# Optimization experiments

Measured on AMD Instinct MI355X. Metric: run time of the kernel, lower is better.

The kernel has to match this reference:

```python
import jax, jax.numpy as jnp
import numpy as np

B, S, HID, H = 1, 2048, 512, 8
D = HID // H            # head_dim = 64
N_TIP, N_FAC = 16, 256
SCALE = 1.0 / np.sqrt(D).astype(np.float32)


def _dominant_dim_indices():
    # dominant_fcs = arange(n_tip) % (head_dim//2), identical for every head
    pair_dim = max(1, D // 2)
    fc = jnp.arange(N_TIP) % pair_dim                      # [n_tip]
    dim_idx = jnp.stack((fc * 2, fc * 2 + 1), axis=-1).reshape(-1)  # [2*n_tip]
    return jnp.clip(dim_idx, 0, D - 1)


def setup_inputs() -> dict:
    key = jax.random.key(0)
    kx, kq, kk, kv, ko = jax.random.split(key, 5)
    s = 1.0 / np.sqrt(HID)
    return {
        "x": jax.random.normal(kx, (B, S, HID), jnp.float32),
        "wq": jax.random.normal(kq, (HID, HID), jnp.float32) * s,
        "wk": jax.random.normal(kk, (HID, HID), jnp.float32) * s,
        "wv": jax.random.normal(kv, (HID, HID), jnp.float32) * s,
        "wo": jax.random.normal(ko, (HID, HID), jnp.float32) * s,
    }


def reference(x, wq, wk, wv, wo):
    # projections (nn.Linear, no bias): y = x @ W.T; split into heads -> [B,H,S,D]
    def split_heads(y):
        return y.reshape(B, S, H, D).transpose(0, 2, 1, 3)

    q = split_heads(x @ wq.T)
    k = split_heads(x @ wk.T)
    v = split_heads(x @ wv.T)

    dim_idx = _dominant_dim_indices()                      # [2*n_tip]
    q_sub = q[..., dim_idx]                                # [B,H,S,2*n_tip]
    k_sub = k[..., dim_idx]
    importance = jnp.einsum("bhqf,bhkf->bhqk", q_sub, k_sub)  # [B,H,S,S]

    n_sel = min(N_FAC, S)
    _, top_idx = jax.lax.top_k(importance, n_sel)          # [B,H,S,n_sel]

    # gather selected K/V per query: [B,H,S,n_sel,D]
    k_sel = jnp.take_along_axis(k[:, :, None], top_idx[..., None], axis=3)
    v_sel = jnp.take_along_axis(v[:, :, None], top_idx[..., None], axis=3)

    scores = jnp.einsum("bhqd,bhqkd->bhqk", q, k_sel) * SCALE
    attn = jax.nn.softmax(scores, axis=-1)
    out = jnp.einsum("bhqk,bhqkd->bhqd", attn, v_sel)      # [B,H,S,D]

    out = out.transpose(0, 2, 1, 3).reshape(B, S, HID)
    return out @ wo.T
```

## Files before the change

### kernel.cpp

```cpp
#include <hip/hip_runtime.h>

#define S_LEN  2048
#define HIDDEN 512
#define NHEAD  8
#define DHEAD  64
#define NSEL   256
#define ROWS_A 8
#define SCALE_ 0.125f

#define WAVE_SYNC() __asm__ volatile("s_waitcnt lgkmcnt(0)" ::: "memory")

__device__ __forceinline__ unsigned mapu(float f) {
  unsigned u = __float_as_uint(f);
  return (u & 0x80000000u) ? ~u : (u | 0x80000000u);
}

union H4 { _Float16 h[4]; uint2 u2; };

__device__ __forceinline__ void gemm_nt_body(const float* __restrict__ A,
                                             const float* __restrict__ B,
                                             float* __restrict__ C,
                                             int K, int N, int m0, int n0,
                                             float (*As)[68], float (*Bs)[68]) {
  const int t  = threadIdx.x;
  const int tx = t & 15, ty = t >> 4;
  const int rr = t >> 3, cc = (t & 7) << 2;
  float acc[4][4] = {};

  float4 fa0 = *(const float4*)&A[(size_t)(m0 + rr)      * K + cc];
  float4 fa1 = *(const float4*)&A[(size_t)(m0 + rr + 32) * K + cc];
  float4 fb0 = *(const float4*)&B[(size_t)(n0 + rr)      * K + cc];
  float4 fb1 = *(const float4*)&B[(size_t)(n0 + rr + 32) * K + cc];

  for (int k0 = 0; k0 < K; k0 += 32) {
    __syncthreads();
    As[cc + 0][rr] = fa0.x; As[cc + 1][rr] = fa0.y; As[cc + 2][rr] = fa0.z; As[cc + 3][rr] = fa0.w;
    As[cc + 0][rr + 32] = fa1.x; As[cc + 1][rr + 32] = fa1.y; As[cc + 2][rr + 32] = fa1.z; As[cc + 3][rr + 32] = fa1.w;
    Bs[cc + 0][rr] = fb0.x; Bs[cc + 1][rr] = fb0.y; Bs[cc + 2][rr] = fb0.z; Bs[cc + 3][rr] = fb0.w;
    Bs[cc + 0][rr + 32] = fb1.x; Bs[cc + 1][rr + 32] = fb1.y; Bs[cc + 2][rr + 32] = fb1.z; Bs[cc + 3][rr + 32] = fb1.w;
    __syncthreads();
    if (k0 + 32 < K) {
      fa0 = *(const float4*)&A[(size_t)(m0 + rr)      * K + k0 + 32 + cc];
      fa1 = *(const float4*)&A[(size_t)(m0 + rr + 32) * K + k0 + 32 + cc];
      fb0 = *(const float4*)&B[(size_t)(n0 + rr)      * K + k0 + 32 + cc];
      fb1 = *(const float4*)&B[(size_t)(n0 + rr + 32) * K + k0 + 32 + cc];
    }
#pragma unroll
    for (int kk = 0; kk < 32; ++kk) {
      const float4 a4 = *(const float4*)&As[kk][ty * 4];
      const float4 b4 = *(const float4*)&Bs[kk][tx * 4];
      const float a[4] = {a4.x, a4.y, a4.z, a4.w};
      const float b[4] = {b4.x, b4.y, b4.z, b4.w};
#pragma unroll
      for (int i = 0; i < 4; ++i)
#pragma unroll
        for (int j = 0; j < 4; ++j) acc[i][j] += a[i] * b[j];
    }
  }
#pragma unroll
  for (int i = 0; i < 4; ++i) {
    float4 o = make_float4(acc[i][0], acc[i][1], acc[i][2], acc[i][3]);
    *(float4*)&C[(size_t)(m0 + ty * 4 + i) * N + n0 + tx * 4] = o;
  }
}

__global__ __launch_bounds__(256) void gemm_nt(const float* __restrict__ A,
                                               const float* __restrict__ B,
                                               float* __restrict__ C,
                                               int M, int N, int K) {
  __shared__ float As[32][68];
  __shared__ float Bs[32][68];
  gemm_nt_body(A, B, C, K, N, blockIdx.x * 64, blockIdx.y * 64, As, Bs);
}

__global__ __launch_bounds__(256) void gemm_qkv(const float* __restrict__ x,
                                                const float* __restrict__ wq,
                                                const float* __restrict__ wk,
                                                const float* __restrict__ wv,
                                                float* __restrict__ Qb,
                                                float* __restrict__ Kb,
                                                float* __restrict__ Vb) {
  __shared__ float As[32][68];
  __shared__ float Bs[32][68];
  const int z = blockIdx.z;
  const float* B = (z == 0) ? wq : (z == 1) ? wk : wv;
  float*       C = (z == 0) ? Qb : (z == 1) ? Kb : Vb;
  gemm_nt_body(x, B, C, HIDDEN, HIDDEN, blockIdx.x * 64, blockIdx.y * 64, As, Bs);
}

__global__ __launch_bounds__(256) void score_gemm(const float* __restrict__ Q,
                                                  const float* __restrict__ K,
                                                  unsigned* __restrict__ impu,
                                                  _Float16* __restrict__ sch) {
  __shared__ float Qs[64][132];
  __shared__ float Ks[64][68];
  const int bid  = blockIdx.x;
  const int h    = bid & (NHEAD - 1);
  const int tile = bid >> 3;
  const int q0   = (tile & 15) * 128;
  const int k0   = (tile >> 4) * 64;
  const int t  = threadIdx.x;
  const int tx = t & 15, ty = t >> 4;

#pragma unroll
  for (int s = 0; s < 8; ++s) {
    const int sf = s * 256 + t;
    const int r = sf >> 4, c = (sf & 15) * 4;
    const float4 f = *(const float4*)&Q[(size_t)(q0 + r) * HIDDEN + h * DHEAD + c];
    Qs[c + 0][r] = f.x; Qs[c + 1][r] = f.y; Qs[c + 2][r] = f.z; Qs[c + 3][r] = f.w;
  }
#pragma unroll
  for (int s = 0; s < 4; ++s) {
    const int sf = s * 256 + t;
    const int r = sf >> 4, c = (sf & 15) * 4;
    const float4 f = *(const float4*)&K[(size_t)(k0 + r) * HIDDEN + h * DHEAD + c];
    Ks[c + 0][r] = f.x; Ks[c + 1][r] = f.y; Ks[c + 2][r] = f.z; Ks[c + 3][r] = f.w;
  }
  __syncthreads();

  float acc[8][4] = {};
#pragma unroll
  for (int d = 0; d < 32; ++d) {
    const float4 aa = *(const float4*)&Qs[d][ty * 8];
    const float4 ab = *(const float4*)&Qs[d][ty * 8 + 4];
    const float4 b4 = *(const float4*)&Ks[d][tx * 4];
    const float a[8] = {aa.x, aa.y, aa.z, aa.w, ab.x, ab.y, ab.z, ab.w};
    const float b[4] = {b4.x, b4.y, b4.z, b4.w};
#pragma unroll
    for (int i = 0; i < 8; ++i)
#pragma unroll
      for (int j = 0; j < 4; ++j) acc[i][j] += a[i] * b[j];
  }
  float simp[8][4];
#pragma unroll
  for (int i = 0; i < 8; ++i)
#pragma unroll
    for (int j = 0; j < 4; ++j) simp[i][j] = acc[i][j];
#pragma unroll
  for (int d = 32; d < 64; ++d) {
    const float4 aa = *(const float4*)&Qs[d][ty * 8];
    const float4 ab = *(const float4*)&Qs[d][ty * 8 + 4];
    const float4 b4 = *(const float4*)&Ks[d][tx * 4];
    const float a[8] = {aa.x, aa.y, aa.z, aa.w, ab.x, ab.y, ab.z, ab.w};
    const float b[4] = {b4.x, b4.y, b4.z, b4.w};
#pragma unroll
    for (int i = 0; i < 8; ++i)
#pragma unroll
      for (int j = 0; j < 4; ++j) acc[i][j] += a[i] * b[j];
  }

#pragma unroll
  for (int i = 0; i < 8; ++i) {
    const size_t gr = (size_t)(h * S_LEN) + q0 + ty * 8 + i;
    const size_t off = gr * S_LEN + k0 + tx * 4;
    *(uint4*)&impu[off] = make_uint4(mapu(simp[i][0]), mapu(simp[i][1]),
                                     mapu(simp[i][2]), mapu(simp[i][3]));
    H4 pk;
#pragma unroll
    for (int j = 0; j < 4; ++j) pk.h[j] = (_Float16)(acc[i][j] * SCALE_);
    *(uint2*)&sch[off] = pk.u2;
  }
}

__global__ __launch_bounds__(512) void fused_select_pv(const unsigned* __restrict__ impu,
                                                       const _Float16* __restrict__ sch,
                                                       const float* __restrict__ V,
                                                       float* __restrict__ AO) {
  __shared__ unsigned hist[ROWS_A][256];
  __shared__ float    sbuf[ROWS_A][NSEL];
  __shared__ unsigned short ibuf[ROWS_A][NSEL];
  __shared__ unsigned short eqbuf[ROWS_A][64];
  __shared__ unsigned rstate[ROWS_A][2];

  const int t = threadIdx.x, wv = t >> 6, lane = t & 63;
  const unsigned long long lmask = (1ull << lane) - 1ull;
  const size_t gr = (size_t)blockIdx.x * ROWS_A + wv;
  const unsigned* rowp  = impu + gr * S_LEN;
  const _Float16* shrow = sch  + gr * S_LEN;

  uint4 u[8];
  H4    s4[8];
#pragma unroll
  for (int j = 0; j < 8; ++j) {
    u[j]     = *(const uint4*)&rowp[j * 256 + lane * 4];
    s4[j].u2 = *(const uint2*)&shrow[j * 256 + lane * 4];
  }

  unsigned prefix = 0, krem = NSEL;
#pragma unroll 1
  for (int b = 3; b >= 0; --b) {
    *(uint4*)&hist[wv][lane * 4] = make_uint4(0u, 0u, 0u, 0u);
    WAVE_SYNC();
    const int shift = b * 8;
#pragma unroll
    for (int j = 0; j < 8; ++j) {
      const unsigned uu[4] = {u[j].x, u[j].y, u[j].z, u[j].w};
#pragma unroll
      for (int e = 0; e < 4; ++e) {
        const unsigned v = uu[e];
        const bool ok = (b == 3) || ((v >> (shift + 8)) == prefix);
        if (ok) atomicAdd(&hist[wv][(v >> shift) & 0xFF], 1u);
      }
    }
    WAVE_SYNC();
    const int g = 63 - lane;
    const uint4 c4 = *(const uint4*)&hist[wv][4 * g];
    const unsigned c0 = c4.x, c1 = c4.y, c2 = c4.z, c3 = c4.w;
    const unsigned lsum = c0 + c1 + c2 + c3;
    unsigned incl = lsum;
#pragma unroll
    for (int off = 1; off < 64; off <<= 1) {
      unsigned o = __shfl_up(incl, off);
      if (lane >= off) incl += o;
    }
    const unsigned excl = incl - lsum;
    const unsigned ab3 = excl, ab2 = excl + c3, ab1 = excl + c3 + c2, ab0 = excl + c3 + c2 + c1;
    if (ab3 < krem && krem <= ab3 + c3) { rstate[wv][0] = 4u*g+3u; rstate[wv][1] = krem - ab3; }
    if (ab2 < krem && krem <= ab2 + c2) { rstate[wv][0] = 4u*g+2u; rstate[wv][1] = krem - ab2; }
    if (ab1 < krem && krem <= ab1 + c1) { rstate[wv][0] = 4u*g+1u; rstate[wv][1] = krem - ab1; }
    if (ab0 < krem && krem <= ab0 + c0) { rstate[wv][0] = 4u*g+0u; rstate[wv][1] = krem - ab0; }
    WAVE_SYNC();
    prefix = (prefix << 8) | rstate[wv][0];
    krem   = rstate[wv][1];
  }
  const unsigned T = prefix;

  unsigned base_gt = 0, base_eq = 0;
#pragma unroll
  for (int j = 0; j < 8; ++j) {
    const unsigned uu[4] = {u[j].x, u[j].y, u[j].z, u[j].w};
#pragma unroll
    for (int e = 0; e < 4; ++e) {
      const unsigned v = uu[e];
      const int i = j * 256 + lane * 4 + e;
      const bool gt = (v > T), eq = (v == T);
      const unsigned long long mg = __ballot(gt);
      const unsigned long long me = __ballot(eq);
      if (gt) {
        const unsigned p = base_gt + (unsigned)__popcll(mg & lmask);
        ibuf[wv][p] = (unsigned short)i;
        sbuf[wv][p] = (float)s4[j].h[e];
      }
      if (eq) {
        const unsigned p = base_eq + (unsigned)__popcll(me & lmask);
        if (p < 64) eqbuf[wv][p] = (unsigned short)i;
      }
      base_gt += (unsigned)__popcll(mg);
      base_eq += (unsigned)__popcll(me);
    }
  }
  WAVE_SYNC();
  const unsigned ngt = base_gt, ne = base_eq;
  const unsigned need = NSEL - ngt;
  if (ne == need && ne <= 64) {
    for (unsigned j = lane; j < ne; j += 64) {
      const unsigned short ix = eqbuf[wv][j];
      ibuf[wv][ngt + j] = ix;
      sbuf[wv][ngt + j] = (float)shrow[ix];
    }
  } else if (lane == 0) {
    if (ne <= 64) {
      for (unsigned j = 0; j < need; ++j) {
        const unsigned short ix = eqbuf[wv][j];
        ibuf[wv][ngt + j] = ix;
        sbuf[wv][ngt + j] = (float)shrow[ix];
      }
    } else {
      unsigned taken = 0;
      for (int i = 0; i < S_LEN && taken < need; ++i)
        if (rowp[i] == T) { ibuf[wv][ngt + taken] = (unsigned short)i; sbuf[wv][ngt + taken] = (float)shrow[i]; ++taken; }
    }
  }
  WAVE_SYNC();

  float sc[4];
#pragma unroll
  for (int m = 0; m < 4; ++m) sc[m] = sbuf[wv][lane * 4 + m];
  float mx = fmaxf(fmaxf(sc[0], sc[1]), fmaxf(sc[2], sc[3]));
#pragma unroll
  for (int off = 32; off; off >>= 1) mx = fmaxf(mx, __shfl_xor(mx, off));
  float zs = 0.f;
#pragma unroll
  for (int m = 0; m < 4; ++m) { sc[m] = expf(sc[m] - mx); zs += sc[m]; }
#pragma unroll
  for (int off = 32; off; off >>= 1) zs += __shfl_xor(zs, off);
  const float rz = 1.0f / zs;
  *(float4*)&sbuf[wv][lane * 4] = make_float4(sc[0], sc[1], sc[2], sc[3]);
  WAVE_SYNC();

  const int h = (int)(gr >> 11), q = (int)(gr & (S_LEN - 1));
  const float* Vh = V + h * DHEAD;
  float outv = 0.f;
#pragma unroll 4
  for (int j = 0; j < NSEL; j += 4) {
    const ushort4 id4 = *(const ushort4*)&ibuf[wv][j];
    const float4  w4  = *(const float4*)&sbuf[wv][j];
    outv += w4.x * Vh[(size_t)id4.x * HIDDEN + lane];
    outv += w4.y * Vh[(size_t)id4.y * HIDDEN + lane];
    outv += w4.z * Vh[(size_t)id4.z * HIDDEN + lane];
    outv += w4.w * Vh[(size_t)id4.w * HIDDEN + lane];
  }
  AO[(size_t)q * HIDDEN + h * DHEAD + lane] = outv * rz;
}

__global__ __launch_bounds__(256) void imp_gemm(const float* __restrict__ Q,
                                                const float* __restrict__ K,
                                                unsigned* __restrict__ impu) {
  __shared__ float Qs[32][68];
  __shared__ float Ks[32][68];
  const int bid  = blockIdx.x;
  const int h    = bid & (NHEAD - 1);
  const int tile = bid >> 3;
  const int q0   = (tile & 31) * 64;
  const int k0   = (tile >> 5) * 64;
  const int t  = threadIdx.x;
  const int tx = t & 15, ty = t >> 4;
#pragma unroll
  for (int s = 0; s < 2; ++s) {
    int slot = t + s * 256;
    int r = slot >> 3, c = (slot & 7) << 2;
    const float4 fq = *(const float4*)&Q[(size_t)(q0 + r) * HIDDEN + h * DHEAD + c];
    Qs[c + 0][r] = fq.x; Qs[c + 1][r] = fq.y; Qs[c + 2][r] = fq.z; Qs[c + 3][r] = fq.w;
    const float4 fk = *(const float4*)&K[(size_t)(k0 + r) * HIDDEN + h * DHEAD + c];
    Ks[c + 0][r] = fk.x; Ks[c + 1][r] = fk.y; Ks[c + 2][r] = fk.z; Ks[c + 3][r] = fk.w;
  }
  __syncthreads();
  float acc[4][4] = {};
#pragma unroll
  for (int d = 0; d < 32; ++d) {
    const float4 a4 = *(const float4*)&Qs[d][ty * 4];
    const float4 b4 = *(const float4*)&Ks[d][tx * 4];
    const float a[4] = {a4.x, a4.y, a4.z, a4.w};
    const float b[4] = {b4.x, b4.y, b4.z, b4.w};
#pragma unroll
    for (int i = 0; i < 4; ++i)
#pragma unroll
      for (int j = 0; j < 4; ++j) acc[i][j] += a[i] * b[j];
  }
#pragma unroll
  for (int i = 0; i < 4; ++i) {
    uint4 o = make_uint4(mapu(acc[i][0]), mapu(acc[i][1]), mapu(acc[i][2]), mapu(acc[i][3]));
    *(uint4*)&impu[((size_t)(h * S_LEN) + q0 + ty * 4 + i) * S_LEN + k0 + tx * 4] = o;
  }
}

__global__ __launch_bounds__(512) void radix_select(const unsigned* __restrict__ impu,
                                                    unsigned short* __restrict__ selg) {
  __shared__ unsigned hist[ROWS_A][256];
  __shared__ unsigned short selbuf[ROWS_A][NSEL];
  __shared__ unsigned short eqbuf[ROWS_A][64];
  __shared__ unsigned cnt[ROWS_A], eqcnt[ROWS_A];
  __shared__ unsigned rstate[ROWS_A][2];

  const int t = threadIdx.x, wv = t >> 6, lane = t & 63;
  const size_t gr = (size_t)blockIdx.x * ROWS_A + wv;
  const unsigned* rowp = impu + gr * S_LEN;

  uint4 u[8];
#pragma unroll
  for (int j = 0; j < 8; ++j) u[j] = *(const uint4*)&rowp[j * 256 + lane * 4];

  unsigned prefix = 0, krem = NSEL;
#pragma unroll 1
  for (int b = 3; b >= 0; --b) {
    hist[wv][lane] = 0; hist[wv][lane + 64] = 0; hist[wv][lane + 128] = 0; hist[wv][lane + 192] = 0;
    WAVE_SYNC();
    const int shift = b * 8;
#pragma unroll
    for (int j = 0; j < 8; ++j) {
      const unsigned uu[4] = {u[j].x, u[j].y, u[j].z, u[j].w};
#pragma unroll
      for (int e = 0; e < 4; ++e) {
        const unsigned v = uu[e];
        const bool ok = (b == 3) || ((v >> (shift + 8)) == prefix);
        if (ok) atomicAdd(&hist[wv][(v >> shift) & 0xFF], 1u);
      }
    }
    WAVE_SYNC();
    const int g = 63 - lane;
    const uint4 c4 = *(const uint4*)&hist[wv][4 * g];
    const unsigned c0 = c4.x, c1 = c4.y, c2 = c4.z, c3 = c4.w;
    const unsigned lsum = c0 + c1 + c2 + c3;
    unsigned incl = lsum;
#pragma unroll
    for (int off = 1; off < 64; off <<= 1) {
      unsigned o = __shfl_up(incl, off);
      if (lane >= off) incl += o;
    }
    const unsigned excl = incl - lsum;
    const unsigned ab3 = excl, ab2 = excl + c3, ab1 = excl + c3 + c2, ab0 = excl + c3 + c2 + c1;
    if (ab3 < krem && krem <= ab3 + c3) { rstate[wv][0] = 4u*g+3u; rstate[wv][1] = krem - ab3; }
    if (ab2 < krem && krem <= ab2 + c2) { rstate[wv][0] = 4u*g+2u; rstate[wv][1] = krem - ab2; }
    if (ab1 < krem && krem <= ab1 + c1) { rstate[wv][0] = 4u*g+1u; rstate[wv][1] = krem - ab1; }
    if (ab0 < krem && krem <= ab0 + c0) { rstate[wv][0] = 4u*g+0u; rstate[wv][1] = krem - ab0; }
    WAVE_SYNC();
    prefix = (prefix << 8) | rstate[wv][0];
    krem   = rstate[wv][1];
  }
  const unsigned T = prefix;

  if (lane == 0) { cnt[wv] = 0; eqcnt[wv] = 0; }
  WAVE_SYNC();
#pragma unroll
  for (int j = 0; j < 8; ++j) {
    const unsigned uu[4] = {u[j].x, u[j].y, u[j].z, u[j].w};
#pragma unroll
    for (int e = 0; e < 4; ++e) {
      const unsigned v = uu[e];
      const int i = j * 256 + lane * 4 + e;
      if (v > T)       { unsigned p = atomicAdd(&cnt[wv], 1u);   selbuf[wv][p] = (unsigned short)i; }
      else if (v == T) { unsigned p = atomicAdd(&eqcnt[wv], 1u); if (p < 64) eqbuf[wv][p] = (unsigned short)i; }
    }
  }
  WAVE_SYNC();
  const unsigned ngt = cnt[wv], ne = eqcnt[wv];
  const unsigned need = NSEL - ngt;
  if (ne == need && ne <= 64) {
    for (unsigned j = lane; j < ne; j += 64) selbuf[wv][ngt + j] = eqbuf[wv][j];
  } else if (lane == 0) {
    if (ne <= 64) {
      for (unsigned a = 1; a < ne; ++a) {
        unsigned short kv = eqbuf[wv][a]; int bp = (int)a;
        while (bp > 0 && eqbuf[wv][bp - 1] > kv) { eqbuf[wv][bp] = eqbuf[wv][bp - 1]; --bp; }
        eqbuf[wv][bp] = kv;
      }
      for (unsigned j = 0; j < need; ++j) selbuf[wv][ngt + j] = eqbuf[wv][j];
    } else {
      unsigned taken = 0;
      for (int i = 0; i < S_LEN && taken < need; ++i)
        if (rowp[i] == T) { selbuf[wv][ngt + taken] = (unsigned short)i; ++taken; }
    }
  }
  WAVE_SYNC();
  if (lane < 32) {
    const uint4 o = *(const uint4*)&selbuf[wv][lane * 8];
    *(uint4*)&selg[gr * NSEL + lane * 8] = o;
  }
}

__global__ __launch_bounds__(256, 4) void fasa_attend(const float* __restrict__ Q,
                                                      const float* __restrict__ K,
                                                      const float* __restrict__ V,
                                                      const unsigned short* __restrict__ selg,
                                                      float* __restrict__ O) {
  __shared__ float qs[4][DHEAD];
  __shared__ float wbuf[4][NSEL];
  __shared__ int   ibuf[4][NSEL];
  const int bid = blockIdx.x;
  const int h   = bid & (NHEAD - 1);
  const int qb  = bid >> 3;
  const int t   = threadIdx.x, wv = t >> 6, lane = t & 63;
  const int row = qb * 4 + wv;

  qs[wv][lane] = Q[(size_t)row * HIDDEN + h * DHEAD + lane];
  const unsigned short* srow = selg + ((size_t)(h * S_LEN) + row) * NSEL;
  const ushort4 s4 = *(const ushort4*)&srow[lane * 4];
  int sidx[4] = {(int)s4.x, (int)s4.y, (int)s4.z, (int)s4.w};
  WAVE_SYNC();

  const float* Kh = K + h * DHEAD;
  float sc[4] = {0.f, 0.f, 0.f, 0.f};
#pragma unroll
  for (int k4 = 0; k4 < 16; ++k4) {
    const float4 qv = *(const float4*)&qs[wv][k4 * 4];
#pragma unroll
    for (int m = 0; m < 4; ++m) {
      const float4 kf = *(const float4*)&Kh[(size_t)sidx[m] * HIDDEN + k4 * 4];
      sc[m] += kf.x * qv.x + kf.y * qv.y + kf.z * qv.z + kf.w * qv.w;
    }
  }
#pragma unroll
  for (int m = 0; m < 4; ++m) sc[m] *= SCALE_;

  float mx = fmaxf(fmaxf(sc[0], sc[1]), fmaxf(sc[2], sc[3]));
#pragma unroll
  for (int off = 32; off; off >>= 1) mx = fmaxf(mx, __shfl_xor(mx, off));
  float zs = 0.f;
#pragma unroll
  for (int m = 0; m < 4; ++m) { sc[m] = expf(sc[m] - mx); zs += sc[m]; }
#pragma unroll
  for (int off = 32; off; off >>= 1) zs += __shfl_xor(zs, off);
  const float rz = 1.0f / zs;

  *(float4*)&wbuf[wv][lane * 4] = make_float4(sc[0], sc[1], sc[2], sc[3]);
  *(int4*)&ibuf[wv][lane * 4]   = make_int4(sidx[0], sidx[1], sidx[2], sidx[3]);
  WAVE_SYNC();

  const float* Vh = V + h * DHEAD;
  float outv = 0.f;
#pragma unroll 4
  for (int j = 0; j < NSEL; j += 4) {
    const int4   id4 = *(const int4*)&ibuf[wv][j];
    const float4 w4  = *(const float4*)&wbuf[wv][j];
    outv += w4.x * Vh[(size_t)id4.x * HIDDEN + lane];
    outv += w4.y * Vh[(size_t)id4.y * HIDDEN + lane];
    outv += w4.z * Vh[(size_t)id4.z * HIDDEN + lane];
    outv += w4.w * Vh[(size_t)id4.w * HIDDEN + lane];
  }
  O[(size_t)row * HIDDEN + h * DHEAD + lane] = outv * rz;
}

extern "C" void kernel_launch(void* const* d_in, const int* in_sizes, int n_in,
                              void* d_out, int out_size, void* d_ws, size_t ws_size,
                              hipStream_t stream) {
  const float* x  = (const float*)d_in[0];
  const float* wq = (const float*)d_in[1];
  const float* wk = (const float*)d_in[2];
  const float* wv = (const float*)d_in[3];
  const float* wo = (const float*)d_in[4];
  float* out = (float*)d_out;

  float* Qb = (float*)d_ws;
  float* Kb = Qb + (size_t)S_LEN * HIDDEN;
  float* Vb = Kb + (size_t)S_LEN * HIDDEN;
  float* AO = Vb + (size_t)S_LEN * HIDDEN;
  void*  tail = (void*)(AO + (size_t)S_LEN * HIDDEN);

  const size_t elems = (size_t)NHEAD * S_LEN * S_LEN;
  const size_t base  = (size_t)4 * S_LEN * HIDDEN * 4;
  const size_t need_new = base + elems * 4 + elems * 2;

  dim3 g(S_LEN / 64, HIDDEN / 64);
  gemm_qkv<<<dim3(S_LEN / 64, HIDDEN / 64, 3), 256, 0, stream>>>(x, wq, wk, wv, Qb, Kb, Vb);
  if (ws_size >= need_new) {
    unsigned* impu = (unsigned*)tail;
    _Float16* sch  = (_Float16*)(impu + elems);
    score_gemm<<<dim3(NHEAD * 16 * 32), 256, 0, stream>>>(Qb, Kb, impu, sch);
    fused_select_pv<<<dim3(NHEAD * S_LEN / ROWS_A), 512, 0, stream>>>(impu, sch, Vb, AO);
  } else {
    unsigned short* selg = (unsigned short*)tail;
    unsigned* impu = (unsigned*)(selg + (size_t)NHEAD * S_LEN * NSEL);
    imp_gemm<<<dim3(NHEAD * 32 * 32), 256, 0, stream>>>(Qb, Kb, impu);
    radix_select<<<dim3(NHEAD * S_LEN / ROWS_A), 512, 0, stream>>>(impu, selg);
    fasa_attend<<<dim3((S_LEN / 4) * NHEAD), 256, 0, stream>>>(Qb, Kb, Vb, selg, AO);
  }
  gemm_nt<<<g, 256, 0, stream>>>(AO, wo, out, S_LEN, HIDDEN, HIDDEN);
}
```

Baseline: 253.2 us.

## Replace 4-pass radix select with value-range histogram and in-wave bucket rank

```diff
diff --git a/kernel.cpp b/kernel.cpp
--- a/kernel.cpp
+++ b/kernel.cpp
@@ -13,6 +13,9 @@
 __device__ __forceinline__ unsigned mapu(float f) {
   unsigned u = __float_as_uint(f);
   return (u & 0x80000000u) ? ~u : (u | 0x80000000u);
+}
+__device__ __forceinline__ float unmapu(unsigned x) {
+  return __uint_as_float((x & 0x80000000u) ? (x & 0x7FFFFFFFu) : ~x);
 }
 
 union H4 { _Float16 h[4]; uint2 u2; };
@@ -168,7 +171,7 @@
                                                        float* __restrict__ AO) {
   __shared__ unsigned hist[ROWS_A][256];
   __shared__ float    sbuf[ROWS_A][NSEL];
-  __shared__ unsigned short ibuf[ROWS_A][NSEL];
+  __shared__ unsigned ibuf[ROWS_A][NSEL];
   __shared__ unsigned short eqbuf[ROWS_A][64];
   __shared__ unsigned rstate[ROWS_A][2];
 
@@ -186,44 +189,196 @@
     s4[j].u2 = *(const uint2*)&shrow[j * 256 + lane * 4];
   }
 
-  unsigned prefix = 0, krem = NSEL;
-#pragma unroll 1
-  for (int b = 3; b >= 0; --b) {
+  unsigned um = u[0].x, uM = u[0].x;
+#pragma unroll
+  for (int j = 0; j < 8; ++j) {
+    um = min(um, min(min(u[j].x, u[j].y), min(u[j].z, u[j].w)));
+    uM = max(uM, max(max(u[j].x, u[j].y), max(u[j].z, u[j].w)));
+  }
+#pragma unroll
+  for (int off = 32; off; off >>= 1) {
+    um = min(um, (unsigned)__shfl_xor((int)um, off));
+    uM = max(uM, (unsigned)__shfl_xor((int)uM, off));
+  }
+
+  unsigned T;
+  if (uM == um) {
+    T = uM;
+  } else {
+    const float vmin  = unmapu(um);
+    const float scale = 255.0f / (unmapu(uM) - vmin);
+
     *(uint4*)&hist[wv][lane * 4] = make_uint4(0u, 0u, 0u, 0u);
     WAVE_SYNC();
-    const int shift = b * 8;
 #pragma unroll
     for (int j = 0; j < 8; ++j) {
       const unsigned uu[4] = {u[j].x, u[j].y, u[j].z, u[j].w};
 #pragma unroll
       for (int e = 0; e < 4; ++e) {
-        const unsigned v = uu[e];
-        const bool ok = (b == 3) || ((v >> (shift + 8)) == prefix);
-        if (ok) atomicAdd(&hist[wv][(v >> shift) & 0xFF], 1u);
+        int bb = (int)((unmapu(uu[e]) - vmin) * scale);
+        bb = bb < 0 ? 0 : (bb > 255 ? 255 : bb);
+        atomicAdd(&hist[wv][bb], 1u);
       }
     }
     WAVE_SYNC();
-    const int g = 63 - lane;
-    const uint4 c4 = *(const uint4*)&hist[wv][4 * g];
-    const unsigned c0 = c4.x, c1 = c4.y, c2 = c4.z, c3 = c4.w;
-    const unsigned lsum = c0 + c1 + c2 + c3;
-    unsigned incl = lsum;
-#pragma unroll
-    for (int off = 1; off < 64; off <<= 1) {
-      unsigned o = __shfl_up(incl, off);
-      if (lane >= off) incl += o;
-    }
-    const unsigned excl = incl - lsum;
-    const unsigned ab3 = excl, ab2 = excl + c3, ab1 = excl + c3 + c2, ab0 = excl + c3 + c2 + c1;
-    if (ab3 < krem && krem <= ab3 + c3) { rstate[wv][0] = 4u*g+3u; rstate[wv][1] = krem - ab3; }
-    if (ab2 < krem && krem <= ab2 + c2) { rstate[wv][0] = 4u*g+2u; rstate[wv][1] = krem - ab2; }
-    if (ab1 < krem && krem <= ab1 + c1) { rstate[wv][0] = 4u*g+1u; rstate[wv][1] = krem - ab1; }
-    if (ab0 < krem && krem <= ab0 + c0) { rstate[wv][0] = 4u*g+0u; rstate[wv][1] = krem - ab0; }
+    {
+      const int g = 63 - lane;
+      const uint4 c4 = *(const uint4*)&hist[wv][4 * g];
+      const unsigned c0 = c4.x, c1 = c4.y, c2 = c4.z, c3 = c4.w;
+      const unsigned lsum = c0 + c1 + c2 + c3;
+      unsigned incl = lsum;
+#pragma unroll
+      for (int off = 1; off < 64; off <<= 1) {
+        unsigned o = __shfl_up(incl, off);
+        if (lane >= off) incl += o;
+      }
+      const unsigned excl = incl - lsum;
+      const unsigned ab3 = excl, ab2 = excl + c3, ab1 = excl + c3 + c2, ab0 = excl + c3 + c2 + c1;
+      if (ab3 < NSEL && NSEL <= ab3 + c3) { rstate[wv][0] = 4u*g+3u; rstate[wv][1] = NSEL - ab3; }
+      if (ab2 < NSEL && NSEL <= ab2 + c2) { rstate[wv][0] = 4u*g+2u; rstate[wv][1] = NSEL - ab2; }
+      if (ab1 < NSEL && NSEL <= ab1 + c1) { rstate[wv][0] = 4u*g+1u; rstate[wv][1] = NSEL - ab1; }
+      if (ab0 < NSEL && NSEL <= ab0 + c0) { rstate[wv][0] = 4u*g+0u; rstate[wv][1] = NSEL - ab0; }
+    }
     WAVE_SYNC();
-    prefix = (prefix << 8) | rstate[wv][0];
-    krem   = rstate[wv][1];
-  }
-  const unsigned T = prefix;
+    const unsigned B    = rstate[wv][0];
+    const unsigned krem = rstate[wv][1];
+    const unsigned nb   = hist[wv][B];
+
+    if (nb <= 64) {
+      unsigned* ebufu = (unsigned*)&sbuf[wv][0];
+      unsigned nbase = 0;
+#pragma unroll
+      for (int j = 0; j < 8; ++j) {
+        const unsigned uu[4] = {u[j].x, u[j].y, u[j].z, u[j].w};
+#pragma unroll
+        for (int e = 0; e < 4; ++e) {
+          const unsigned x = uu[e];
+          int bb = (int)((unmapu(x) - vmin) * scale);
+          bb = bb < 0 ? 0 : (bb > 255 ? 255 : bb);
+          const bool inb = (bb == (int)B);
+          const unsigned long long m = __ballot(inb);
+          if (inb) ebufu[nbase + (unsigned)__popcll(m & lmask)] = x;
+          nbase += (unsigned)__popcll(m);
+        }
+      }
+      WAVE_SYNC();
+      const unsigned myv = (lane < (int)nb) ? ebufu[lane] : 0u;
+      unsigned gtc = 0, eqc = 0;
+      for (unsigned jj = 0; jj < nb; ++jj) {
+        const unsigned bv = (unsigned)__shfl((int)myv, (int)jj);
+        gtc += (bv > myv) ? 1u : 0u;
+        eqc += (bv == myv) ? 1u : 0u;
+      }
+      if (lane < (int)nb && gtc < krem && krem <= gtc + eqc) rstate[wv][0] = myv;
+      WAVE_SYNC();
+      T = rstate[wv][0];
+    } else {
+      unsigned m2min = 0xFFFFFFFFu, m2max = 0u;
+      for (int i = lane; i < S_LEN; i += 64) {
+        const unsigned x = rowp[i];
+        int bb = (int)((unmapu(x) - vmin) * scale);
+        bb = bb < 0 ? 0 : (bb > 255 ? 255 : bb);
+        if (bb == (int)B) { m2min = min(m2min, x); m2max = max(m2max, x); }
+      }
+#pragma unroll
+      for (int off = 32; off; off >>= 1) {
+        m2min = min(m2min, (unsigned)__shfl_xor((int)m2min, off));
+        m2max = max(m2max, (unsigned)__shfl_xor((int)m2max, off));
+      }
+      if (m2max == m2min) {
+        T = m2max;
+      } else {
+        const float vlo2   = unmapu(m2min);
+        const float scale2 = 255.0f / (unmapu(m2max) - vlo2);
+        *(uint4*)&hist[wv][lane * 4] = make_uint4(0u, 0u, 0u, 0u);
+        WAVE_SYNC();
+        for (int i = lane; i < S_LEN; i += 64) {
+          const unsigned x = rowp[i];
+          const float v = unmapu(x);
+          int bb = (int)((v - vmin) * scale);
+          bb = bb < 0 ? 0 : (bb > 255 ? 255 : bb);
+          if (bb == (int)B) {
+            int b2 = (int)((v - vlo2) * scale2);
+            b2 = b2 < 0 ? 0 : (b2 > 255 ? 255 : b2);
+            atomicAdd(&hist[wv][b2], 1u);
+          }
+        }
+        WAVE_SYNC();
+        {
+          const int g = 63 - lane;
+          const uint4 c4 = *(const uint4*)&hist[wv][4 * g];
+          const unsigned c0 = c4.x, c1 = c4.y, c2 = c4.z, c3 = c4.w;
+          const unsigned lsum = c0 + c1 + c2 + c3;
+          unsigned incl = lsum;
+#pragma unroll
+          for (int off = 1; off < 64; off <<= 1) {
+            unsigned o = __shfl_up(incl, off);
+            if (lane >= off) incl += o;
+          }
+          const unsigned excl = incl - lsum;
+          const unsigned ab3 = excl, ab2 = excl + c3, ab1 = excl + c3 + c2, ab0 = excl + c3 + c2 + c1;
+          if (ab3 < krem && krem <= ab3 + c3) { rstate[wv][0] = 4u*g+3u; rstate[wv][1] = krem - ab3; }
+          if (ab2 < krem && krem <= ab2 + c2) { rstate[wv][0] = 4u*g+2u; rstate[wv][1] = krem - ab2; }
+          if (ab1 < krem && krem <= ab1 + c1) { rstate[wv][0] = 4u*g+1u; rstate[wv][1] = krem - ab1; }
+          if (ab0 < krem && krem <= ab0 + c0) { rstate[wv][0] = 4u*g+0u; rstate[wv][1] = krem - ab0; }
+        }
+        WAVE_SYNC();
+        const unsigned B2    = rstate[wv][0];
+        const unsigned krem2 = rstate[wv][1];
+        const unsigned nb2   = hist[wv][B2];
+        if (nb2 <= 64) {
+          unsigned* ebufu = (unsigned*)&sbuf[wv][0];
+          unsigned nbase = 0;
+          for (int i = lane; i < S_LEN; i += 64) {
+            const unsigned x = rowp[i];
+            const float v = unmapu(x);
+            int bb = (int)((v - vmin) * scale);
+            bb = bb < 0 ? 0 : (bb > 255 ? 255 : bb);
+            bool inb = false;
+            if (bb == (int)B) {
+              int b2 = (int)((v - vlo2) * scale2);
+              b2 = b2 < 0 ? 0 : (b2 > 255 ? 255 : b2);
+              inb = (b2 == (int)B2);
+            }
+            const unsigned long long m = __ballot(inb);
+            if (inb) ebufu[nbase + (unsigned)__popcll(m & lmask)] = x;
+            nbase += (unsigned)__popcll(m);
+          }
+          WAVE_SYNC();
+          const unsigned myv = (lane < (int)nb2) ? ebufu[lane] : 0u;
+          unsigned gtc = 0, eqc = 0;
+          for (unsigned jj = 0; jj < nb2; ++jj) {
+            const unsigned bv = (unsigned)__shfl((int)myv, (int)jj);
+            gtc += (bv > myv) ? 1u : 0u;
+            eqc += (bv == myv) ? 1u : 0u;
+          }
+          if (lane < (int)nb2 && gtc < krem2 && krem2 <= gtc + eqc) rstate[wv][0] = myv;
+          WAVE_SYNC();
+          T = rstate[wv][0];
+        } else {
+          if (lane == 0) {
+            unsigned pfx = 0, kr = NSEL;
+            for (int rb = 3; rb >= 0; --rb) {
+              for (int i2 = 0; i2 < 256; ++i2) hist[wv][i2] = 0u;
+              for (int i2 = 0; i2 < S_LEN; ++i2) {
+                const unsigned x = rowp[i2];
+                if (rb == 3 || ((x >> (rb * 8 + 8)) == pfx)) hist[wv][(x >> (rb * 8)) & 0xFF]++;
+              }
+              unsigned cum = 0, sel = 0;
+              for (int bb2 = 255; bb2 >= 0; --bb2) {
+                if (kr <= cum + hist[wv][bb2]) { sel = (unsigned)bb2; kr -= cum; break; }
+                cum += hist[wv][bb2];
+              }
+              pfx = (pfx << 8) | sel;
+            }
+            rstate[wv][0] = pfx;
+          }
+          WAVE_SYNC();
+          T = rstate[wv][0];
+        }
+      }
+    }
+  }
 
   unsigned base_gt = 0, base_eq = 0;
 #pragma unroll
@@ -238,7 +393,7 @@
       const unsigned long long me = __ballot(eq);
       if (gt) {
         const unsigned p = base_gt + (unsigned)__popcll(mg & lmask);
-        ibuf[wv][p] = (unsigned short)i;
+        ibuf[wv][p] = (unsigned)i << 9;
         sbuf[wv][p] = (float)s4[j].h[e];
       }
       if (eq) {
@@ -255,20 +410,20 @@
   if (ne == need && ne <= 64) {
     for (unsigned j = lane; j < ne; j += 64) {
       const unsigned short ix = eqbuf[wv][j];
-      ibuf[wv][ngt + j] = ix;
+      ibuf[wv][ngt + j] = (unsigned)ix << 9;
       sbuf[wv][ngt + j] = (float)shrow[ix];
     }
   } else if (lane == 0) {
     if (ne <= 64) {
       for (unsigned j = 0; j < need; ++j) {
         const unsigned short ix = eqbuf[wv][j];
-        ibuf[wv][ngt + j] = ix;
+        ibuf[wv][ngt + j] = (unsigned)ix << 9;
         sbuf[wv][ngt + j] = (float)shrow[ix];
       }
     } else {
       unsigned taken = 0;
       for (int i = 0; i < S_LEN && taken < need; ++i)
-        if (rowp[i] == T) { ibuf[wv][ngt + taken] = (unsigned short)i; sbuf[wv][ngt + taken] = (float)shrow[i]; ++taken; }
+        if (rowp[i] == T) { ibuf[wv][ngt + taken] = (unsigned)i << 9; sbuf[wv][ngt + taken] = (float)shrow[i]; ++taken; }
     }
   }
   WAVE_SYNC();
@@ -289,16 +444,16 @@
   WAVE_SYNC();
 
   const int h = (int)(gr >> 11), q = (int)(gr & (S_LEN - 1));
-  const float* Vh = V + h * DHEAD;
+  const float* Vhl = V + h * DHEAD + lane;
   float outv = 0.f;
 #pragma unroll 4
   for (int j = 0; j < NSEL; j += 4) {
-    const ushort4 id4 = *(const ushort4*)&ibuf[wv][j];
-    const float4  w4  = *(const float4*)&sbuf[wv][j];
-    outv += w4.x * Vh[(size_t)id4.x * HIDDEN + lane];
-    outv += w4.y * Vh[(size_t)id4.y * HIDDEN + lane];
-    outv += w4.z * Vh[(size_t)id4.z * HIDDEN + lane];
-    outv += w4.w * Vh[(size_t)id4.w * HIDDEN + lane];
+    const uint4  id4 = *(const uint4*)&ibuf[wv][j];
+    const float4 w4  = *(const float4*)&sbuf[wv][j];
+    outv += w4.x * Vhl[id4.x];
+    outv += w4.y * Vhl[id4.y];
+    outv += w4.z * Vhl[id4.z];
+    outv += w4.w * Vhl[id4.w];
   }
   AO[(size_t)q * HIDDEN + h * DHEAD + lane] = outv * rz;
 }
```

Result: faster. 227.2 us (-10.3%).
